# Optimization experiments

Measured on AMD Instinct MI355X. Metric: run time of the kernel, lower is better.

The kernel has to match this reference:

```python
import jax, jax.numpy as jnp
import numpy as np

B, C_IN, T, V = 32, 64, 300, 25
C_OUT = 128
INTER = max(8, C_IN // 2)
EPS = 1e-5


def setup_inputs() -> dict:
    key = jax.random.key(0)
    ks = jax.random.split(key, 9)
    s_in = 1.0 / np.sqrt(C_IN)
    return {
        "x": jax.random.normal(ks[0], (B, C_IN, T, V), dtype=jnp.float32),
        "theta_w": jax.random.uniform(ks[1], (INTER, C_IN), jnp.float32, -s_in, s_in),
        "theta_b": jax.random.uniform(ks[2], (INTER,), jnp.float32, -s_in, s_in),
        "phi_w": jax.random.uniform(ks[3], (INTER, C_IN), jnp.float32, -s_in, s_in),
        "phi_b": jax.random.uniform(ks[4], (INTER,), jnp.float32, -s_in, s_in),
        "g_w": jax.random.uniform(ks[5], (C_OUT, C_IN), jnp.float32, -s_in, s_in),
        "g_b": jax.random.uniform(ks[6], (C_OUT,), jnp.float32, -s_in, s_in),
        "bn_gamma": jnp.ones((C_OUT,), jnp.float32),
        "bn_beta": jnp.zeros((C_OUT,), jnp.float32),
    }


def reference(x, theta_w, theta_b, phi_w, phi_b, g_w, g_b, bn_gamma, bn_beta):
    # 1x1 convs == per-position linear projections over the channel dim
    th = jnp.einsum("bctv,ic->btvi", x, theta_w) + theta_b      # (B,T,V,inter)
    ph = jnp.einsum("bctv,ic->btiv", x, phi_w) + phi_b[None, None, :, None]  # (B,T,inter,V)
    # small-V non-local attention, per (b,t) slice
    scale = 1.0 / jnp.sqrt(jnp.asarray(INTER, x.dtype))
    A = jax.nn.softmax(jnp.einsum("btvi,btiw->btvw", th, ph) * scale, axis=-1)  # (B,T,V,V)
    g = jnp.einsum("bctv,oc->btvo", x, g_w) + g_b               # (B,T,V,out)
    out = jnp.einsum("btvw,btwo->btvo", A, g)                    # (B,T,V,out)
    out = jnp.transpose(out, (0, 3, 1, 2))                       # (B,out,T,V)
    # BatchNorm2d in training mode: batch stats over (B,T,V), biased variance
    mean = jnp.mean(out, axis=(0, 2, 3), keepdims=True)
    var = jnp.var(out, axis=(0, 2, 3), keepdims=True)
    out = (out - mean) * jax.lax.rsqrt(var + EPS)
    out = out * bn_gamma[None, :, None, None] + bn_beta[None, :, None, None]
    return out
```

## Files before the change

kernel.cpp:

```cpp
#include <hip/hip_runtime.h>

#define NB 32
#define CIN 64
#define TT 300
#define VV 25
#define CO 128
#define NSLICE 9600
#define NBLK 2400
#define NBUCKET 64
#define EPSV 1e-5f
#define SCALEV 0.17677669529663687f
#define NRED (NB*TT*VV)

using bf16x8 = __attribute__((ext_vector_type(8))) short;
using f32x4  = __attribute__((ext_vector_type(4))) float;
using f32x16 = __attribute__((ext_vector_type(16))) float;
typedef unsigned short ushort_t;

__device__ __forceinline__ unsigned short f2bf(float f) {
    union { float f; unsigned u; } v; v.f = f;
    unsigned u = v.u;
    return (unsigned short)((u + 0x7fffu + ((u >> 16) & 1u)) >> 16);
}

__device__ __forceinline__ unsigned pkbf(float a, float b) {
    unsigned r;
    asm("v_cvt_pk_bf16_f32 %0, %1, %2" : "=v"(r) : "v"(a), "v"(b));
    return r;
}

__device__ __forceinline__ void plswap(unsigned &a, unsigned &b) {
#if __has_builtin(__builtin_amdgcn_permlane32_swap)
    auto r = __builtin_amdgcn_permlane32_swap(a, b, false, false);
    a = r[0]; b = r[1];
#else
    unsigned a2, b2;
    asm("v_permlane32_swap_b32 %0, %1" : "=v"(a2), "=v"(b2) : "0"(a), "1"(b));
    a = a2; b = b2;
#endif
}
__device__ __forceinline__ float xhalf_sum(float x) {
    unsigned a = __float_as_uint(x), b = __float_as_uint(x);
    plswap(a, b);
    return __uint_as_float(a) + __uint_as_float(b);
}
__device__ __forceinline__ float xhalf_max(float x) {
    unsigned a = __float_as_uint(x), b = __float_as_uint(x);
    plswap(a, b);
    return fmaxf(__uint_as_float(a), __uint_as_float(b));
}
__device__ __forceinline__ f32x16 splat16(float v) {
    f32x16 r;
    #pragma unroll
    for (int i = 0; i < 16; ++i) r[i] = v;
    return r;
}

__device__ __forceinline__ void rearr(const f32x16& d, bf16x8& f0, bf16x8& f1) {
    unsigned u0 = pkbf(d[0],  d[1]),  u1 = pkbf(d[2],  d[3]);
    unsigned u2 = pkbf(d[4],  d[5]),  u3 = pkbf(d[6],  d[7]);
    unsigned u4 = pkbf(d[8],  d[9]),  u5 = pkbf(d[10], d[11]);
    unsigned u6 = pkbf(d[12], d[13]), u7 = pkbf(d[14], d[15]);
    plswap(u0, u2); plswap(u1, u3); plswap(u4, u6); plswap(u5, u7);
    union { unsigned u[4]; bf16x8 v; } c0, c1;
    c0.u[0] = u0; c0.u[1] = u1; c0.u[2] = u2; c0.u[3] = u3;
    c1.u[0] = u4; c1.u[1] = u5; c1.u[2] = u6; c1.u[3] = u7;
    f0 = c0.v; f1 = c1.v;
}

__global__ void agc_k0(const float* __restrict__ tw, const float* __restrict__ pw,
                       const float* __restrict__ gw,
                       const float* __restrict__ tb, const float* __restrict__ pb,
                       ushort_t* __restrict__ twA, ushort_t* __restrict__ pwA,
                       ushort_t* __restrict__ gwB,
                       float* __restrict__ tbD, float* __restrict__ pbD)
{
    int e = blockIdx.x*256 + threadIdx.x;
    if (e < 12288) {
        int j = e & 7, l = (e >> 3) & 63, ks = (e >> 9) & 3;
        int c = ks*16 + (l >> 5)*8 + j;
        int n = l & 31;
        int grp = e >> 11;
        if (grp == 0)      twA[e]        = f2bf(tw[n*CIN + c]);
        else if (grp == 1) pwA[e - 2048] = f2bf(pw[n*CIN + c]);
        else               gwB[e - 4096] = f2bf(gw[(grp - 2)*32*CIN + n*CIN + c]);
    } else if (e < 14336) {
        int e2 = e - 12288;
        int r = e2 & 15, l = (e2 >> 4) & 63;
        int i = (r & 3) + 8*(r >> 2) + 4*(l >> 5);
        if (e2 < 1024) tbD[e2]        = tb[i];
        else           pbD[e2 - 1024] = pb[i];
    }
}

__global__ __launch_bounds__(256) void agc_k1(
    const float* __restrict__ x, const float* __restrict__ gb,
    const ushort_t* __restrict__ twA, const ushort_t* __restrict__ pwA,
    const ushort_t* __restrict__ gwB,
    const float* __restrict__ tbD, const float* __restrict__ pbD,
    float* __restrict__ out, float* __restrict__ bsum, float* __restrict__ bsq)
{
    __shared__ __align__(16) float lds[7680];
    float* xs   = lds;
    float* outS = lds;
    float* red  = lds + 7424;

    const int tid  = threadIdx.x;
    const int lane = tid & 63;
    const int wid  = tid >> 6;
    const int l31  = lane & 31;
    const int h    = lane >> 5;

    const int blk = blockIdx.x;
    const int grp = (blk & 7) * (NBLK/8) + (blk >> 3);
    const int b   = grp / 75;
    const int j4  = grp - b*75;

    red[tid] = 0.f;

    const float4* gx = (const float4*)x + (size_t)b*120000 + (size_t)j4*25;
    for (int e = tid; e < 1600; e += 256) {
        int c = e / 25, q = e - c*25;
        *(float4*)&xs[c*100 + q*4] = gx[(size_t)c*1875 + q];
    }
    __syncthreads();

    const int vcl  = l31 < VV ? l31 : VV-1;
    const int colx = wid*25 + vcl;
    bf16x8 xf[4];
    #pragma unroll
    for (int ks = 0; ks < 4; ++ks) {
        float v[8];
        #pragma unroll
        for (int j = 0; j < 8; ++j)
            v[j] = xs[(ks*16 + h*8 + j)*100 + colx];
        union { unsigned u[4]; bf16x8 f; } c;
        c.u[0] = pkbf(v[0], v[1]); c.u[1] = pkbf(v[2], v[3]);
        c.u[2] = pkbf(v[4], v[5]); c.u[3] = pkbf(v[6], v[7]);
        xf[ks] = c.f;
    }
    __syncthreads();

    f32x16 th, ph;
    #pragma unroll
    for (int r = 0; r < 4; ++r) {
        f32x4 bb = ((const f32x4*)(tbD + lane*16))[r];
        th[4*r+0] = bb[0]; th[4*r+1] = bb[1]; th[4*r+2] = bb[2]; th[4*r+3] = bb[3];
        f32x4 pp = ((const f32x4*)(pbD + lane*16))[r];
        ph[4*r+0] = pp[0]; ph[4*r+1] = pp[1]; ph[4*r+2] = pp[2]; ph[4*r+3] = pp[3];
    }
    #pragma unroll
    for (int ks = 0; ks < 4; ++ks) {
        bf16x8 twf = *(const bf16x8*)(twA + (ks*64 + lane)*8);
        th = __builtin_amdgcn_mfma_f32_32x32x16_bf16(twf, xf[ks], th, 0, 0, 0);
        bf16x8 pwf = *(const bf16x8*)(pwA + (ks*64 + lane)*8);
        ph = __builtin_amdgcn_mfma_f32_32x32x16_bf16(pwf, xf[ks], ph, 0, 0, 0);
    }

    bf16x8 thf0, thf1, phf0, phf1;
    rearr(th, thf0, thf1);
    rearr(ph, phf0, phf1);
    f32x16 st = splat16(0.f);
    st = __builtin_amdgcn_mfma_f32_32x32x16_bf16(phf0, thf0, st, 0, 0, 0);
    st = __builtin_amdgcn_mfma_f32_32x32x16_bf16(phf1, thf1, st, 0, 0, 0);

    float s[13];
    #pragma unroll
    for (int r = 0; r < 13; ++r) s[r] = st[r] * SCALEV;
    float m = fmaxf(fmaxf(fmaxf(s[0], s[1]), fmaxf(s[2], s[3])),
                    fmaxf(fmaxf(s[4], s[5]), fmaxf(s[6], s[7])));
    m = fmaxf(m, fmaxf(fmaxf(s[8], s[9]), fmaxf(s[10], s[11])));
    float s12 = h ? -3.4e38f : s[12];
    m = fmaxf(m, s12);
    m = xhalf_max(m);
    f32x16 pd;
    #pragma unroll
    for (int r = 0; r < 12; ++r) pd[r] = __expf(s[r] - m);
    pd[12] = h ? 0.f : __expf(s[12] - m);
    pd[13] = 0.f; pd[14] = 0.f; pd[15] = 0.f;
    float sum = ((pd[0]+pd[1]) + (pd[2]+pd[3])) + ((pd[4]+pd[5]) + (pd[6]+pd[7]))
              + ((pd[8]+pd[9]) + (pd[10]+pd[11])) + pd[12];
    sum = xhalf_sum(sum);
    float rinv;
    asm("v_rcp_f32 %0, %1" : "=v"(rinv) : "v"(sum));
    #pragma unroll
    for (int r = 0; r < 13; ++r) pd[r] *= rinv;
    bf16x8 pf0, pf1;
    rearr(pd, pf0, pf1);

    auto process_ot = [&](int ot) {
        f32x16 gd = splat16(0.f);
        #pragma unroll
        for (int ks = 0; ks < 4; ++ks) {
            bf16x8 gf = *(const bf16x8*)(gwB + ((ot*4 + ks)*64 + lane)*8);
            gd = __builtin_amdgcn_mfma_f32_32x32x16_bf16(xf[ks], gf, gd, 0, 0, 0);
        }
        bf16x8 gf0, gf1;
        rearr(gd, gf0, gf1);
        f32x16 od = splat16(gb[ot*32 + l31]);
        od = __builtin_amdgcn_mfma_f32_32x32x16_bf16(pf0, gf0, od, 0, 0, 0);
        od = __builtin_amdgcn_mfma_f32_32x32x16_bf16(pf1, gf1, od, 0, 0, 0);

        const int o_loc = (ot & 1)*32 + l31;
        float* base = &outS[o_loc*116 + wid*28];
        float ss = 0.f, qq = 0.f;
        #pragma unroll
        for (int q = 0; q < 3; ++q) {
            f32x4 qv = {od[4*q], od[4*q+1], od[4*q+2], od[4*q+3]};
            *(f32x4*)&base[8*q + 4*h] = qv;
            ss += (qv[0] + qv[1]) + (qv[2] + qv[3]);
            qq = fmaf(qv[0], qv[0], qq); qq = fmaf(qv[1], qv[1], qq);
            qq = fmaf(qv[2], qv[2], qq); qq = fmaf(qv[3], qv[3], qq);
        }
        if (!h) {
            base[24] = od[12];
            ss += od[12]; qq = fmaf(od[12], od[12], qq);
        }
        ss = xhalf_sum(ss); qq = xhalf_sum(qq);
        if (lane < 32) {
            atomicAdd(&red[ot*32 + l31], ss);
            atomicAdd(&red[128 + ot*32 + l31], qq);
        }
    };

    auto readback = [&](int p) {
        for (int e = tid; e < 1600; e += 256) {
            int o_loc = e / 25, q2 = e - o_loc*25;
            int v0 = 4*q2;
            const float* row = &outS[o_loc*116];
            float tmp[4];
            #pragma unroll
            for (int jj = 0; jj < 4; ++jj) {
                int v = v0 + jj;
                int sdx = (v*41) >> 10;
                tmp[jj] = row[v + 3*sdx];
            }
            float4 val;
            val.x = tmp[0]; val.y = tmp[1]; val.z = tmp[2]; val.w = tmp[3];
            ((float4*)out)[(size_t)(b*CO + p*64 + o_loc)*1875 + (size_t)j4*25 + q2] = val;
        }
    };

    process_ot(0); process_ot(1);
    __syncthreads();
    readback(0);
    __syncthreads();
    process_ot(2); process_ot(3);
    __syncthreads();
    readback(1);
    if (tid < CO) {
        int bkt = blk & (NBUCKET-1);
        atomicAdd(&bsum[bkt*CO + tid], red[tid]);
        atomicAdd(&bsq [bkt*CO + tid], red[128 + tid]);
    }
}

__global__ void agc_k2(const float* __restrict__ bsum, const float* __restrict__ bsq,
                       const float* __restrict__ gamma, const float* __restrict__ beta,
                       float* __restrict__ scl, float* __restrict__ shf)
{
    const int o = threadIdx.x;
    float s = 0.f, q = 0.f;
    for (int k = 0; k < NBUCKET; ++k) { s += bsum[k*CO + o]; q += bsq[k*CO + o]; }
    float mean = s / (float)NRED;
    float var  = q / (float)NRED - mean*mean;
    float rstd = rsqrtf(var + EPSV);
    float sc = gamma[o] * rstd;
    scl[o] = sc;
    shf[o] = beta[o] - mean * sc;
}

__global__ __launch_bounds__(256) void agc_k3(
    float* __restrict__ out, const float* __restrict__ scl, const float* __restrict__ shf)
{
    const int n4 = NB*CO*TT*VV/4;
    float4* p = (float4*)out;
    for (int i = blockIdx.x*blockDim.x + threadIdx.x; i < n4; i += gridDim.x*blockDim.x) {
        int ch = (i / (TT*VV/4)) & (CO-1);
        float4 v = p[i];
        float sc = scl[ch], sh = shf[ch];
        v.x = fmaf(v.x, sc, sh);
        v.y = fmaf(v.y, sc, sh);
        v.z = fmaf(v.z, sc, sh);
        v.w = fmaf(v.w, sc, sh);
        p[i] = v;
    }
}

extern "C" void kernel_launch(void* const* d_in, const int* in_sizes, int n_in,
                              void* d_out, int out_size, void* d_ws, size_t ws_size,
                              hipStream_t stream) {
    const float* x     = (const float*)d_in[0];
    const float* tw    = (const float*)d_in[1];
    const float* tbb   = (const float*)d_in[2];
    const float* pw    = (const float*)d_in[3];
    const float* pbb   = (const float*)d_in[4];
    const float* gw    = (const float*)d_in[5];
    const float* gbb   = (const float*)d_in[6];
    const float* gamma = (const float*)d_in[7];
    const float* beta  = (const float*)d_in[8];
    float* out = (float*)d_out;
    float* ws  = (float*)d_ws;

    float* bsum = ws;
    float* bsq  = ws + NBUCKET*CO;
    float* scl  = ws + 2*NBUCKET*CO;
    float* shf  = ws + 2*NBUCKET*CO + CO;
    ushort_t* twA = (ushort_t*)(ws + 2*NBUCKET*CO + 2*CO);
    ushort_t* pwA = twA + 2048;
    ushort_t* gwB = twA + 4096;
    float* tbD = (float*)(gwB + 8192);
    float* pbD = tbD + 1024;

    hipMemsetAsync(d_ws, 0, (size_t)(2*NBUCKET*CO)*sizeof(float), stream);
    agc_k0<<<56, 256, 0, stream>>>(tw, pw, gw, tbb, pbb, twA, pwA, gwB, tbD, pbD);
    agc_k1<<<NBLK, 256, 0, stream>>>(x, gbb, twA, pwA, gwB, tbD, pbD, out, bsum, bsq);
    agc_k2<<<1, CO, 0, stream>>>(bsum, bsq, gamma, beta, scl, shf);
    agc_k3<<<2048, 256, 0, stream>>>(out, scl, shf);
}
```

Measured before the change: 98.16 us.

## Stage output in bf16 LDS, preload g weights, fuse workspace zeroing

Stores the per-block output tile in LDS as bf16 instead of fp32, while computing BN statistics from the fp32 accumulators. The g weight fragments for two output tiles are loaded up front, so their global loads overlap before the MFMA chains. The workspace memset is merged into the weight-prep kernel to drop one launch. The cost is extra rounding of the pre-BN output to bf16 and a changed LDS allocation size.

Result: faster. 96.22 us (-2.0%).

```diff
diff --git a/kernel.cpp b/kernel.cpp
--- a/kernel.cpp
+++ b/kernel.cpp
@@ -22,13 +22,11 @@
     unsigned u = v.u;
     return (unsigned short)((u + 0x7fffu + ((u >> 16) & 1u)) >> 16);
 }
-
 __device__ __forceinline__ unsigned pkbf(float a, float b) {
     unsigned r;
     asm("v_cvt_pk_bf16_f32 %0, %1, %2" : "=v"(r) : "v"(a), "v"(b));
     return r;
 }
-
 __device__ __forceinline__ void plswap(unsigned &a, unsigned &b) {
 #if __has_builtin(__builtin_amdgcn_permlane32_swap)
     auto r = __builtin_amdgcn_permlane32_swap(a, b, false, false);
@@ -55,7 +53,6 @@
     for (int i = 0; i < 16; ++i) r[i] = v;
     return r;
 }
-
 __device__ __forceinline__ void rearr(const f32x16& d, bf16x8& f0, bf16x8& f1) {
     unsigned u0 = pkbf(d[0],  d[1]),  u1 = pkbf(d[2],  d[3]);
     unsigned u2 = pkbf(d[4],  d[5]),  u3 = pkbf(d[6],  d[7]);
@@ -73,9 +70,11 @@
                        const float* __restrict__ tb, const float* __restrict__ pb,
                        ushort_t* __restrict__ twA, ushort_t* __restrict__ pwA,
                        ushort_t* __restrict__ gwB,
-                       float* __restrict__ tbD, float* __restrict__ pbD)
+                       float* __restrict__ tbD, float* __restrict__ pbD,
+                       float* __restrict__ zws)
 {
     int e = blockIdx.x*256 + threadIdx.x;
+    if (e < 16384) zws[e] = 0.f;
     if (e < 12288) {
         int j = e & 7, l = (e >> 3) & 63, ks = (e >> 9) & 3;
         int c = ks*16 + (l >> 5)*8 + j;
@@ -100,10 +99,10 @@
     const float* __restrict__ tbD, const float* __restrict__ pbD,
     float* __restrict__ out, float* __restrict__ bsum, float* __restrict__ bsq)
 {
-    __shared__ __align__(16) float lds[7680];
-    float* xs   = lds;
-    float* outS = lds;
-    float* red  = lds + 7424;
+    __shared__ __align__(16) unsigned char ldsb[26624];
+    float* xs       = (float*)ldsb;
+    ushort_t* outSb = (ushort_t*)ldsb;
+    float* red      = (float*)(ldsb + 25600);
 
     const int tid  = threadIdx.x;
     const int lane = tid & 63;
@@ -188,13 +187,11 @@
     bf16x8 pf0, pf1;
     rearr(pd, pf0, pf1);
 
-    auto process_ot = [&](int ot) {
+    auto process_ot = [&](int ot, const bf16x8* gfp) {
         f32x16 gd = splat16(0.f);
         #pragma unroll
-        for (int ks = 0; ks < 4; ++ks) {
-            bf16x8 gf = *(const bf16x8*)(gwB + ((ot*4 + ks)*64 + lane)*8);
-            gd = __builtin_amdgcn_mfma_f32_32x32x16_bf16(xf[ks], gf, gd, 0, 0, 0);
-        }
+        for (int ks = 0; ks < 4; ++ks)
+            gd = __builtin_amdgcn_mfma_f32_32x32x16_bf16(xf[ks], gfp[ks], gd, 0, 0, 0);
         bf16x8 gf0, gf1;
         rearr(gd, gf0, gf1);
         f32x16 od = splat16(gb[ot*32 + l31]);
@@ -202,18 +199,21 @@
         od = __builtin_amdgcn_mfma_f32_32x32x16_bf16(pf1, gf1, od, 0, 0, 0);
 
         const int o_loc = (ot & 1)*32 + l31;
-        float* base = &outS[o_loc*116 + wid*28];
+        ushort_t* base = &outSb[o_loc*116 + wid*28];
         float ss = 0.f, qq = 0.f;
         #pragma unroll
         for (int q = 0; q < 3; ++q) {
-            f32x4 qv = {od[4*q], od[4*q+1], od[4*q+2], od[4*q+3]};
-            *(f32x4*)&base[8*q + 4*h] = qv;
-            ss += (qv[0] + qv[1]) + (qv[2] + qv[3]);
-            qq = fmaf(qv[0], qv[0], qq); qq = fmaf(qv[1], qv[1], qq);
-            qq = fmaf(qv[2], qv[2], qq); qq = fmaf(qv[3], qv[3], qq);
+            unsigned u0 = pkbf(od[4*q],   od[4*q+1]);
+            unsigned u1 = pkbf(od[4*q+2], od[4*q+3]);
+            *(uint2*)&base[8*q + 4*h] = make_uint2(u0, u1);
+            ss += (od[4*q] + od[4*q+1]) + (od[4*q+2] + od[4*q+3]);
+            qq = fmaf(od[4*q],   od[4*q],   qq);
+            qq = fmaf(od[4*q+1], od[4*q+1], qq);
+            qq = fmaf(od[4*q+2], od[4*q+2], qq);
+            qq = fmaf(od[4*q+3], od[4*q+3], qq);
         }
         if (!h) {
-            base[24] = od[12];
+            base[24] = f2bf(od[12]);
             ss += od[12]; qq = fmaf(od[12], od[12], qq);
         }
         ss = xhalf_sum(ss); qq = xhalf_sum(qq);
@@ -227,13 +227,13 @@
         for (int e = tid; e < 1600; e += 256) {
             int o_loc = e / 25, q2 = e - o_loc*25;
             int v0 = 4*q2;
-            const float* row = &outS[o_loc*116];
+            const ushort_t* row = &outSb[o_loc*116];
             float tmp[4];
             #pragma unroll
             for (int jj = 0; jj < 4; ++jj) {
                 int v = v0 + jj;
                 int sdx = (v*41) >> 10;
-                tmp[jj] = row[v + 3*sdx];
+                tmp[jj] = __uint_as_float(((unsigned)row[v + 3*sdx]) << 16);
             }
             float4 val;
             val.x = tmp[0]; val.y = tmp[1]; val.z = tmp[2]; val.w = tmp[3];
@@ -241,11 +241,22 @@
         }
     };
 
-    process_ot(0); process_ot(1);
+    bf16x8 gA[4], gB_[4];
+    #pragma unroll
+    for (int ks = 0; ks < 4; ++ks) {
+        gA[ks]  = *(const bf16x8*)(gwB + ((0*4 + ks)*64 + lane)*8);
+        gB_[ks] = *(const bf16x8*)(gwB + ((1*4 + ks)*64 + lane)*8);
+    }
+    process_ot(0, gA); process_ot(1, gB_);
     __syncthreads();
     readback(0);
     __syncthreads();
-    process_ot(2); process_ot(3);
+    #pragma unroll
+    for (int ks = 0; ks < 4; ++ks) {
+        gA[ks]  = *(const bf16x8*)(gwB + ((2*4 + ks)*64 + lane)*8);
+        gB_[ks] = *(const bf16x8*)(gwB + ((3*4 + ks)*64 + lane)*8);
+    }
+    process_ot(2, gA); process_ot(3, gB_);
     __syncthreads();
     readback(1);
     if (tid < CO) {
@@ -312,8 +323,7 @@
     float* tbD = (float*)(gwB + 8192);
     float* pbD = tbD + 1024;
 
-    hipMemsetAsync(d_ws, 0, (size_t)(2*NBUCKET*CO)*sizeof(float), stream);
-    agc_k0<<<56, 256, 0, stream>>>(tw, pw, gw, tbb, pbb, twA, pwA, gwB, tbD, pbD);
+    agc_k0<<<64, 256, 0, stream>>>(tw, pw, gw, tbb, pbb, twA, pwA, gwB, tbD, pbD, ws);
     agc_k1<<<NBLK, 256, 0, stream>>>(x, gbb, twA, pwA, gwB, tbD, pbD, out, bsum, bsq);
     agc_k2<<<1, CO, 0, stream>>>(bsum, bsq, gamma, beta, scl, shf);
     agc_k3<<<2048, 256, 0, stream>>>(out, scl, shf);
```
